# Performance work log

Measured on AMD Instinct MI355X. Metric: run time of the kernel, lower is better.

## Reference

```python
import jax, jax.numpy as jnp
import numpy as np

DIM = 128
EPS = 1e-5  # torch LayerNorm default


def setup_inputs() -> dict:
    key = jax.random.key(0)
    ks = jax.random.split(key, 8)
    N = 262144
    x = jax.random.normal(ks[0], (N, DIM), dtype=jnp.float32)
    # Parameters (stored as [in, out] for jax matmul); scale ~ torch default init
    ln_w = jnp.ones((DIM,), dtype=jnp.float32)
    ln_b = jnp.zeros((DIM,), dtype=jnp.float32)
    s1 = 1.0 / np.sqrt(DIM)
    s2 = 1.0 / np.sqrt(2 * DIM)
    w1 = jax.random.uniform(ks[1], (DIM, 2 * DIM), jnp.float32, -s1, s1)
    b1 = jax.random.uniform(ks[2], (2 * DIM,), jnp.float32, -s1, s1)
    w2 = jax.random.uniform(ks[3], (2 * DIM, DIM), jnp.float32, -s2, s2)
    b2 = jax.random.uniform(ks[4], (2 * DIM,), jnp.float32, -s2, s2)[:DIM]
    wg = jax.random.uniform(ks[5], (2 * DIM, DIM), jnp.float32, -s2, s2)
    bg = jax.random.uniform(ks[6], (DIM,), jnp.float32, -s2, s2)
    return {"x": x, "ln_w": ln_w, "ln_b": ln_b, "w1": w1, "b1": b1,
            "w2": w2, "b2": b2, "wg": wg, "bg": bg, "passes": 8}


def reference(x, ln_w, ln_b, w1, b1, w2, b2, wg, bg, passes):
    # Split the gate weight so we avoid materializing the concat [state, refined].
    wg_s, wg_r = wg[:DIM], wg[DIM:]

    def step(state, _):
        mu = jnp.mean(state, axis=-1, keepdims=True)
        var = jnp.mean(jnp.square(state - mu), axis=-1, keepdims=True)
        h = (state - mu) * jax.lax.rsqrt(var + EPS) * ln_w + ln_b
        refined = jax.nn.gelu(h @ w1 + b1, approximate=False) @ w2 + b2
        gate = jax.nn.sigmoid(state @ wg_s + refined @ wg_r + bg)
        return state + gate * refined, None

    state, _ = jax.lax.scan(step, x, None, length=passes)
    return state
```

## Files before the change

### kernel.cpp

```cpp
#include <hip/hip_runtime.h>
#include <math.h>

#define DIM 128
#define HID 256
#define MT 64
#define NT 512
#define H_STRIDE 136
#define G_STRIDE 264
#define D_STRIDE 132

typedef __attribute__((ext_vector_type(8))) short bf16x8;
typedef __attribute__((ext_vector_type(4))) float f32x4;
typedef __attribute__((ext_vector_type(4))) unsigned int u32x4;

#define MFMA(a, b, c) __builtin_amdgcn_mfma_f32_16x16x32_bf16((a), (b), (c), 0, 0, 0)

__device__ __forceinline__ unsigned int pack2(float lo, float hi) {
    unsigned int a = __float_as_uint(lo) + 0x8000u;
    unsigned int b = __float_as_uint(hi) + 0x8000u;
    return __builtin_amdgcn_perm(b, a, 0x07060302u);
}
__device__ __forceinline__ unsigned short rb16(float f) {
    return (unsigned short)((__float_as_uint(f) + 0x8000u) >> 16);
}
__device__ __forceinline__ float frcp(float x) { return __builtin_amdgcn_rcpf(x); }
__device__ __forceinline__ float ex2(float x)  { return __builtin_amdgcn_exp2f(x); }
__device__ __forceinline__ float gelu_f(float t) {
    const float u = t * fmaf(t * t, -0.1029436f, -2.3022082f);
    return t * frcp(1.f + ex2(u));
}
__device__ __forceinline__ float sigm(float x) { return frcp(1.f + ex2(-1.442695f * x)); }
__device__ __forceinline__ f32x4 splat4(float v) { f32x4 r = {v, v, v, v}; return r; }

__global__ void w2g_setup(const float* __restrict__ w2, const float* __restrict__ wg,
                          const float* __restrict__ b2, const float* __restrict__ bg,
                          float* __restrict__ w2g)
{
    __shared__ float wr[DIM][DIM + 1];
    const int t = threadIdx.x;
    for (int i = t; i < DIM * DIM; i += 256)
        wr[i >> 7][i & 127] = wg[DIM * DIM + i];
    __syncthreads();
    const int row = blockIdx.x * 32 + (t >> 3);
    const int c0  = (t & 7) * 16;
    float acc[16];
#pragma unroll
    for (int j = 0; j < 16; ++j) acc[j] = 0.f;
    for (int k = 0; k < DIM; ++k) {
        const float a = w2[row * DIM + k];
#pragma unroll
        for (int j = 0; j < 16; ++j) acc[j] = fmaf(a, wr[k][c0 + j], acc[j]);
    }
#pragma unroll
    for (int j = 0; j < 16; ++j) w2g[row * DIM + c0 + j] = acc[j];
    if (blockIdx.x == 0 && t < DIM) {
        float s = bg[t];
        for (int k = 0; k < DIM; ++k) s = fmaf(b2[k], wr[k][t], s);
        w2g[256 * DIM + t] = s;
    }
}

__global__ __launch_bounds__(NT) void trw_kernel(
    const float* __restrict__ x,
    const float* __restrict__ ln_w, const float* __restrict__ ln_b,
    const float* __restrict__ w1, const float* __restrict__ b1,
    const float* __restrict__ w2, const float* __restrict__ b2,
    const float* __restrict__ wg,
    const float* __restrict__ w2g,
    const int* __restrict__ passes_p,
    float* __restrict__ out, int nrows)
{
    __shared__ __align__(16) unsigned short hBuf[MT * H_STRIDE];
    __shared__ __align__(16) unsigned short gBuf[MT * G_STRIDE];
    __shared__ __align__(16) float dBuf[MT * D_STRIDE];
    __shared__ __align__(16) float muB[MT];
    __shared__ __align__(16) float sgB[MT];
    unsigned int* gBuf32 = (unsigned int*)gBuf;

    const int tid = threadIdx.x;
    const int w = tid >> 6, l = tid & 63, q = l >> 4, c16 = l & 15;
    const int hrow = tid >> 3;
    const int hcg  = (tid & 7) << 4;
    const int np = passes_p[0];

    const int colA = 32 * w + c16, colB = colA + 16, colG = 16 * w + c16;
    bf16x8 w1f[2][4], wgsf[4];
#pragma unroll
    for (int kk = 0; kk < 4; ++kk) {
        bf16x8 fa, fb, fg;
#pragma unroll
        for (int j = 0; j < 8; ++j) {
            const int k = kk * 32 + q * 8 + j;
            const float lwk = ln_w[k];
            fa[j] = (short)rb16(lwk * w1[k * HID + colA]);
            fb[j] = (short)rb16(lwk * w1[k * HID + colB]);
            fg[j] = (short)rb16(wg[k * DIM + colG]);
        }
        w1f[0][kk] = fa; w1f[1][kk] = fb; wgsf[kk] = fg;
    }
    bf16x8 w2f[8], w2gf[8];
#pragma unroll
    for (int kk = 0; kk < 8; ++kk) {
        bf16x8 f2, fg;
#pragma unroll
        for (int j = 0; j < 8; ++j) {
            const int p  = kk * 32 + q * 8 + j;
            const int p5 = p & 31;
            const int L  = (p & ~31) + ((p5 & 1) << 4) + (p5 >> 1);
            f2[j] = (short)rb16(w2[L * DIM + colG]);
            fg[j] = (short)rb16(w2g[L * DIM + colG]);
        }
        w2f[kk] = f2; w2gf[kk] = fg;
    }
    float b1vA = b1[colA], b1vB = b1[colB], cs1 = 0.f;
    for (int k = 0; k < DIM; ++k) {
        const float lbk = ln_b[k];
        b1vA = fmaf(lbk, w1[k * HID + colA], b1vA);
        b1vB = fmaf(lbk, w1[k * HID + colB], b1vB);
        cs1 += wg[k * DIM + colG];
    }
    const float b2v = b2[colG];
    const float bgv = w2g[256 * DIM + colG];

    const int nTiles = nrows / MT;
    for (int tile = blockIdx.x; tile < nTiles; tile += gridDim.x) {
        float st[16];
        {
            const float* xr = x + (size_t)(tile * MT + hrow) * DIM + hcg;
#pragma unroll
            for (int v = 0; v < 4; ++v) {
                f32x4 a = *(const f32x4*)(xr + 4 * v);
#pragma unroll
                for (int j = 0; j < 4; ++j) st[4 * v + j] = a[j];
            }
        }

        for (int p = 0; p < np; ++p) {
            if (p > 0) {
#pragma unroll
                for (int v = 0; v < 4; ++v) {
                    f32x4 d = *(f32x4*)&dBuf[hrow * D_STRIDE + hcg + 4 * v];
#pragma unroll
                    for (int j = 0; j < 4; ++j) st[4 * v + j] += d[j];
                }
            }
            float s1 = 0.f, s2 = 0.f;
#pragma unroll
            for (int j = 0; j < 16; ++j) { s1 += st[j]; s2 = fmaf(st[j], st[j], s2); }
#pragma unroll
            for (int m = 4; m >= 1; m >>= 1) { s1 += __shfl_xor(s1, m); s2 += __shfl_xor(s2, m); }
            const float mu = s1 * (1.f / DIM);
            const float ve = fmaf(-mu, mu, s2 * (1.f / DIM)) + 1e-5f;
            const float rs = rsqrtf(ve);
            const float sg = ve * rs;
            const float mrs = mu * rs;
            unsigned int hp[8];
#pragma unroll
            for (int j = 0; j < 8; ++j)
                hp[j] = pack2(fmaf(st[2 * j], rs, -mrs), fmaf(st[2 * j + 1], rs, -mrs));
            u32x4 h0 = {hp[0], hp[1], hp[2], hp[3]}, h1 = {hp[4], hp[5], hp[6], hp[7]};
            *(u32x4*)&hBuf[hrow * H_STRIDE + hcg]     = h0;
            *(u32x4*)&hBuf[hrow * H_STRIDE + hcg + 8] = h1;
            if ((tid & 7) == 0) { muB[hrow] = mu; sgB[hrow] = sg; }
            __syncthreads();

            f32x4 acc0[4], acc1[4], accg[4];
#pragma unroll
            for (int rt = 0; rt < 4; ++rt) {
                acc0[rt] = splat4(b1vA); acc1[rt] = splat4(b1vB); accg[rt] = splat4(0.f);
            }
#pragma unroll
            for (int rt = 0; rt < 4; ++rt)
#pragma unroll
                for (int kk = 0; kk < 4; ++kk) {
                    bf16x8 a = *(bf16x8*)&hBuf[(rt * 16 + c16) * H_STRIDE + kk * 32 + q * 8];
                    acc0[rt] = MFMA(a, w1f[0][kk], acc0[rt]);
                    acc1[rt] = MFMA(a, w1f[1][kk], acc1[rt]);
                    accg[rt] = MFMA(a, wgsf[kk], accg[rt]);
                }
#pragma unroll
            for (int rt = 0; rt < 4; ++rt) {
                f32x4 muv = *(f32x4*)&muB[rt * 16 + q * 4];
                f32x4 sgv = *(f32x4*)&sgB[rt * 16 + q * 4];
#pragma unroll
                for (int r = 0; r < 4; ++r) {
                    const int row = rt * 16 + q * 4 + r;
                    gBuf32[row * (G_STRIDE / 2) + 16 * w + c16] =
                        pack2(gelu_f(acc0[rt][r]), gelu_f(acc1[rt][r]));
                    accg[rt][r] = fmaf(sgv[r], accg[rt][r], muv[r] * cs1);
                }
            }
            __syncthreads();

            f32x4 acc2[4], accr[4];
#pragma unroll
            for (int rt = 0; rt < 4; ++rt) { acc2[rt] = splat4(b2v); accr[rt] = splat4(bgv); }
#pragma unroll
            for (int rt = 0; rt < 4; ++rt)
#pragma unroll
                for (int kk = 0; kk < 8; ++kk) {
                    bf16x8 a = *(bf16x8*)&gBuf[(rt * 16 + c16) * G_STRIDE + kk * 32 + q * 8];
                    acc2[rt] = MFMA(a, w2f[kk], acc2[rt]);
                    accr[rt] = MFMA(a, w2gf[kk], accr[rt]);
                }
#pragma unroll
            for (int rt = 0; rt < 4; ++rt)
#pragma unroll
                for (int r = 0; r < 4; ++r) {
                    const int row = rt * 16 + q * 4 + r;
                    const float gate = sigm(accg[rt][r] + accr[rt][r]);
                    dBuf[row * D_STRIDE + 16 * w + c16] = gate * acc2[rt][r];
                }
            __syncthreads();
        }

        {
            float* orow = out + (size_t)(tile * MT + hrow) * DIM + hcg;
#pragma unroll
            for (int v = 0; v < 4; ++v) {
                f32x4 d = *(f32x4*)&dBuf[hrow * D_STRIDE + hcg + 4 * v];
                f32x4 o;
#pragma unroll
                for (int j = 0; j < 4; ++j) o[j] = st[4 * v + j] + d[j];
                *(f32x4*)(orow + 4 * v) = o;
            }
        }
    }
}

extern "C" void kernel_launch(void* const* d_in, const int* in_sizes, int n_in,
                              void* d_out, int out_size, void* d_ws, size_t ws_size,
                              hipStream_t stream) {
    const float* x    = (const float*)d_in[0];
    const float* ln_w = (const float*)d_in[1];
    const float* ln_b = (const float*)d_in[2];
    const float* w1   = (const float*)d_in[3];
    const float* b1   = (const float*)d_in[4];
    const float* w2   = (const float*)d_in[5];
    const float* b2   = (const float*)d_in[6];
    const float* wg   = (const float*)d_in[7];
    const float* bg   = (const float*)d_in[8];
    const int* passes = (const int*)d_in[9];
    float* out = (float*)d_out;
    float* w2g = (float*)d_ws;

    const int nrows = in_sizes[0] / DIM;
    hipLaunchKernelGGL(w2g_setup, dim3(8), dim3(256), 0, stream, w2, wg, b2, bg, w2g);
    hipLaunchKernelGGL(trw_kernel, dim3(1024), dim3(NT), 0, stream,
                       x, ln_w, ln_b, w1, b1, w2, b2, wg, w2g, passes, out, nrows);
}
```

Baseline: 959.6 us.

## Split row tile into two half-tiles and software-pipeline LN/GEMM phases

Splits each 64-row tile into two 32-row halves and interleaves their stages, so one half's LayerNorm or second GEMM runs between the same barriers as the other half's first GEMM. The aim is to fill MFMA idle time around barriers and cut the number of serialized phases per pass. The cost is more complex control flow and a different thread-to-row mapping (16 threads per row with a wider shuffle reduction). It also adds register pressure, since gate partials for both halves stay live across stages.

```diff
diff --git a/kernel.cpp b/kernel.cpp
--- a/kernel.cpp
+++ b/kernel.cpp
@@ -79,8 +79,8 @@
 
     const int tid = threadIdx.x;
     const int w = tid >> 6, l = tid & 63, q = l >> 4, c16 = l & 15;
-    const int hrow = tid >> 3;
-    const int hcg  = (tid & 7) << 4;
+    const int r16 = tid >> 4;
+    const int hc  = (tid & 15) << 3;
     const int np = passes_p[0];
 
     const int colA = 32 * w + c16, colB = colA + 16, colG = 16 * w + c16;
@@ -122,110 +122,142 @@
     const float b2v = b2[colG];
     const float bgv = w2g[256 * DIM + colG];
 
+#define HUB(S, ADD)                                                                     \
+    {                                                                                   \
+        if (ADD) {                                                                      \
+            _Pragma("unroll")                                                           \
+            for (int v = 0; v < 2; ++v) {                                               \
+                f32x4 d = *(f32x4*)&dBuf[((S)*32 + r16) * D_STRIDE + hc + 4 * v];       \
+                _Pragma("unroll")                                                       \
+                for (int j = 0; j < 4; ++j) st##S[4 * v + j] += d[j];                   \
+            }                                                                           \
+        }                                                                               \
+        float s1 = 0.f, s2 = 0.f;                                                       \
+        _Pragma("unroll")                                                               \
+        for (int j = 0; j < 8; ++j) { s1 += st##S[j]; s2 = fmaf(st##S[j], st##S[j], s2); } \
+        _Pragma("unroll")                                                               \
+        for (int m = 8; m >= 1; m >>= 1) { s1 += __shfl_xor(s1, m); s2 += __shfl_xor(s2, m); } \
+        const float mu = s1 * (1.f / DIM);                                              \
+        const float ve = fmaf(-mu, mu, s2 * (1.f / DIM)) + 1e-5f;                       \
+        const float rs = rsqrtf(ve);                                                    \
+        const float sg = ve * rs;                                                       \
+        const float mrs = mu * rs;                                                      \
+        unsigned int hp[4];                                                             \
+        _Pragma("unroll")                                                               \
+        for (int j = 0; j < 4; ++j)                                                     \
+            hp[j] = pack2(fmaf(st##S[2 * j], rs, -mrs), fmaf(st##S[2 * j + 1], rs, -mrs)); \
+        u32x4 hv = {hp[0], hp[1], hp[2], hp[3]};                                        \
+        *(u32x4*)&hBuf[((S)*32 + r16) * H_STRIDE + hc] = hv;                            \
+        if ((tid & 15) == 0) { muB[(S)*32 + r16] = mu; sgB[(S)*32 + r16] = sg; }        \
+    }
+
+#define M1E1(S, GS)                                                                     \
+    {                                                                                   \
+        f32x4 acc0[2], acc1[2], accg[2];                                                \
+        _Pragma("unroll")                                                               \
+        for (int rt = 0; rt < 2; ++rt) {                                                \
+            acc0[rt] = splat4(b1vA); acc1[rt] = splat4(b1vB); accg[rt] = splat4(0.f);   \
+        }                                                                               \
+        _Pragma("unroll")                                                               \
+        for (int rt = 0; rt < 2; ++rt)                                                  \
+            _Pragma("unroll")                                                           \
+            for (int kk = 0; kk < 4; ++kk) {                                            \
+                bf16x8 a = *(bf16x8*)&hBuf[((S)*32 + rt * 16 + c16) * H_STRIDE + kk * 32 + q * 8]; \
+                acc0[rt] = MFMA(a, w1f[0][kk], acc0[rt]);                               \
+                acc1[rt] = MFMA(a, w1f[1][kk], acc1[rt]);                               \
+                accg[rt] = MFMA(a, wgsf[kk], accg[rt]);                                 \
+            }                                                                           \
+        _Pragma("unroll")                                                               \
+        for (int rt = 0; rt < 2; ++rt) {                                                \
+            f32x4 muv = *(f32x4*)&muB[(S)*32 + rt * 16 + q * 4];                        \
+            f32x4 sgv = *(f32x4*)&sgB[(S)*32 + rt * 16 + q * 4];                        \
+            _Pragma("unroll")                                                           \
+            for (int r = 0; r < 4; ++r) {                                               \
+                const int row = (S)*32 + rt * 16 + q * 4 + r;                           \
+                gBuf32[row * (G_STRIDE / 2) + 16 * w + c16] =                           \
+                    pack2(gelu_f(acc0[rt][r]), gelu_f(acc1[rt][r]));                    \
+                GS[rt][r] = fmaf(sgv[r], accg[rt][r], muv[r] * cs1);                    \
+            }                                                                           \
+        }                                                                               \
+    }
+
+#define M2E2(S, GS)                                                                     \
+    {                                                                                   \
+        f32x4 acc2[2], accr[2];                                                         \
+        _Pragma("unroll")                                                               \
+        for (int rt = 0; rt < 2; ++rt) { acc2[rt] = splat4(b2v); accr[rt] = splat4(bgv); } \
+        _Pragma("unroll")                                                               \
+        for (int rt = 0; rt < 2; ++rt)                                                  \
+            _Pragma("unroll")                                                           \
+            for (int kk = 0; kk < 8; ++kk) {                                            \
+                bf16x8 a = *(bf16x8*)&gBuf[((S)*32 + rt * 16 + c16) * G_STRIDE + kk * 32 + q * 8]; \
+                acc2[rt] = MFMA(a, w2f[kk], acc2[rt]);                                  \
+                accr[rt] = MFMA(a, w2gf[kk], accr[rt]);                                 \
+            }                                                                           \
+        _Pragma("unroll")                                                               \
+        for (int rt = 0; rt < 2; ++rt)                                                  \
+            _Pragma("unroll")                                                           \
+            for (int r = 0; r < 4; ++r) {                                               \
+                const int row = (S)*32 + rt * 16 + q * 4 + r;                           \
+                const float gate = sigm(GS[rt][r] + accr[rt][r]);                       \
+                dBuf[row * D_STRIDE + 16 * w + c16] = gate * acc2[rt][r];               \
+            }                                                                           \
+    }
+
+#define FIN(S)                                                                          \
+    {                                                                                   \
+        float* orow = out + (size_t)(tile * MT + (S)*32 + r16) * DIM + hc;              \
+        _Pragma("unroll")                                                               \
+        for (int v = 0; v < 2; ++v) {                                                   \
+            f32x4 d = *(f32x4*)&dBuf[((S)*32 + r16) * D_STRIDE + hc + 4 * v];           \
+            f32x4 o;                                                                    \
+            _Pragma("unroll")                                                           \
+            for (int j = 0; j < 4; ++j) o[j] = st##S[4 * v + j] + d[j];                 \
+            *(f32x4*)(orow + 4 * v) = o;                                                \
+        }                                                                               \
+    }
+
     const int nTiles = nrows / MT;
     for (int tile = blockIdx.x; tile < nTiles; tile += gridDim.x) {
-        float st[16];
+        float st0[8], st1[8];
         {
-            const float* xr = x + (size_t)(tile * MT + hrow) * DIM + hcg;
-#pragma unroll
-            for (int v = 0; v < 4; ++v) {
-                f32x4 a = *(const f32x4*)(xr + 4 * v);
-#pragma unroll
-                for (int j = 0; j < 4; ++j) st[4 * v + j] = a[j];
+            const float* xr0 = x + (size_t)(tile * MT + r16) * DIM + hc;
+            const float* xr1 = xr0 + 32 * DIM;
+#pragma unroll
+            for (int v = 0; v < 2; ++v) {
+                f32x4 a0 = *(const f32x4*)(xr0 + 4 * v);
+                f32x4 a1 = *(const f32x4*)(xr1 + 4 * v);
+#pragma unroll
+                for (int j = 0; j < 4; ++j) { st0[4 * v + j] = a0[j]; st1[4 * v + j] = a1[j]; }
             }
         }
 
+        f32x4 gsA[2], gsB[2];
+
+        HUB(1, false)
+        __syncthreads();
+
         for (int p = 0; p < np; ++p) {
-            if (p > 0) {
-#pragma unroll
-                for (int v = 0; v < 4; ++v) {
-                    f32x4 d = *(f32x4*)&dBuf[hrow * D_STRIDE + hcg + 4 * v];
-#pragma unroll
-                    for (int j = 0; j < 4; ++j) st[4 * v + j] += d[j];
-                }
+            M1E1(1, gsB)
+            HUB(0, (p > 0))
+            __syncthreads();
+            M2E2(1, gsB)
+            M1E1(0, gsA)
+            __syncthreads();
+            if (p < np - 1) {
+                HUB(1, true)
+            } else {
+                FIN(1)
             }
-            float s1 = 0.f, s2 = 0.f;
-#pragma unroll
-            for (int j = 0; j < 16; ++j) { s1 += st[j]; s2 = fmaf(st[j], st[j], s2); }
-#pragma unroll
-            for (int m = 4; m >= 1; m >>= 1) { s1 += __shfl_xor(s1, m); s2 += __shfl_xor(s2, m); }
-            const float mu = s1 * (1.f / DIM);
-            const float ve = fmaf(-mu, mu, s2 * (1.f / DIM)) + 1e-5f;
-            const float rs = rsqrtf(ve);
-            const float sg = ve * rs;
-            const float mrs = mu * rs;
-            unsigned int hp[8];
-#pragma unroll
-            for (int j = 0; j < 8; ++j)
-                hp[j] = pack2(fmaf(st[2 * j], rs, -mrs), fmaf(st[2 * j + 1], rs, -mrs));
-            u32x4 h0 = {hp[0], hp[1], hp[2], hp[3]}, h1 = {hp[4], hp[5], hp[6], hp[7]};
-            *(u32x4*)&hBuf[hrow * H_STRIDE + hcg]     = h0;
-            *(u32x4*)&hBuf[hrow * H_STRIDE + hcg + 8] = h1;
-            if ((tid & 7) == 0) { muB[hrow] = mu; sgB[hrow] = sg; }
+            M2E2(0, gsA)
             __syncthreads();
-
-            f32x4 acc0[4], acc1[4], accg[4];
-#pragma unroll
-            for (int rt = 0; rt < 4; ++rt) {
-                acc0[rt] = splat4(b1vA); acc1[rt] = splat4(b1vB); accg[rt] = splat4(0.f);
-            }
-#pragma unroll
-            for (int rt = 0; rt < 4; ++rt)
-#pragma unroll
-                for (int kk = 0; kk < 4; ++kk) {
-                    bf16x8 a = *(bf16x8*)&hBuf[(rt * 16 + c16) * H_STRIDE + kk * 32 + q * 8];
-                    acc0[rt] = MFMA(a, w1f[0][kk], acc0[rt]);
-                    acc1[rt] = MFMA(a, w1f[1][kk], acc1[rt]);
-                    accg[rt] = MFMA(a, wgsf[kk], accg[rt]);
-                }
-#pragma unroll
-            for (int rt = 0; rt < 4; ++rt) {
-                f32x4 muv = *(f32x4*)&muB[rt * 16 + q * 4];
-                f32x4 sgv = *(f32x4*)&sgB[rt * 16 + q * 4];
-#pragma unroll
-                for (int r = 0; r < 4; ++r) {
-                    const int row = rt * 16 + q * 4 + r;
-                    gBuf32[row * (G_STRIDE / 2) + 16 * w + c16] =
-                        pack2(gelu_f(acc0[rt][r]), gelu_f(acc1[rt][r]));
-                    accg[rt][r] = fmaf(sgv[r], accg[rt][r], muv[r] * cs1);
-                }
-            }
-            __syncthreads();
-
-            f32x4 acc2[4], accr[4];
-#pragma unroll
-            for (int rt = 0; rt < 4; ++rt) { acc2[rt] = splat4(b2v); accr[rt] = splat4(bgv); }
-#pragma unroll
-            for (int rt = 0; rt < 4; ++rt)
-#pragma unroll
-                for (int kk = 0; kk < 8; ++kk) {
-                    bf16x8 a = *(bf16x8*)&gBuf[(rt * 16 + c16) * G_STRIDE + kk * 32 + q * 8];
-                    acc2[rt] = MFMA(a, w2f[kk], acc2[rt]);
-                    accr[rt] = MFMA(a, w2gf[kk], accr[rt]);
-                }
-#pragma unroll
-            for (int rt = 0; rt < 4; ++rt)
-#pragma unroll
-                for (int r = 0; r < 4; ++r) {
-                    const int row = rt * 16 + q * 4 + r;
-                    const float gate = sigm(accg[rt][r] + accr[rt][r]);
-                    dBuf[row * D_STRIDE + 16 * w + c16] = gate * acc2[rt][r];
-                }
-            __syncthreads();
-        }
-
-        {
-            float* orow = out + (size_t)(tile * MT + hrow) * DIM + hcg;
-#pragma unroll
-            for (int v = 0; v < 4; ++v) {
-                f32x4 d = *(f32x4*)&dBuf[hrow * D_STRIDE + hcg + 4 * v];
-                f32x4 o;
-#pragma unroll
-                for (int j = 0; j < 4; ++j) o[j] = st[4 * v + j] + d[j];
-                *(f32x4*)(orow + 4 * v) = o;
-            }
-        }
-    }
+        }
+        FIN(0)
+    }
+#undef HUB
+#undef M1E1
+#undef M2E2
+#undef FIN
 }
 
 extern "C" void kernel_launch(void* const* d_in, const int* in_sizes, int n_in,
```

New measurement: 964.8 us. No clear change (+0.5%).
